# Kernel tuning notes

Measured on AMD Instinct MI355X. Metric: run time of the kernel, lower is better.

The kernel has to match this reference:

```python
import jax, jax.numpy as jnp
import numpy as np

BPTT, BSZ, NTOKEN = 32, 32, 2000
NINP, NHID = 1024, 256


def setup_inputs() -> dict:
    key = jax.random.key(0)
    ks = jax.random.split(key, 8)
    s = 0.1  # matches uniform(-0.1, 0.1) init scale
    return {
        "input": jax.random.normal(ks[0], (BPTT, BSZ, NTOKEN), jnp.float32),
        "b": jax.random.normal(ks[1], (BSZ, NHID), jnp.float32),
        "RBF_w": jax.random.uniform(ks[2], (NINP, NTOKEN), jnp.float32, -s, s),
        "RBF_b": jnp.zeros((NINP,), jnp.float32),
        "emb_w": jax.random.uniform(ks[3], (NHID, NINP), jnp.float32, -s, s),
        "emb_b": jnp.zeros((NHID,), jnp.float32),
        "wfef_w": jax.random.uniform(ks[4], (NHID * NHID, NHID), jnp.float32, -s, s),
        "wfef_b": jnp.zeros((NHID * NHID,), jnp.float32),
        "dec_w": jax.random.uniform(ks[5], (NTOKEN, NHID), jnp.float32, -s, s),
        "dec_b": jnp.zeros((NTOKEN,), jnp.float32),
    }


def reference(input, b, RBF_w, RBF_b, emb_w, emb_b, wfef_w, wfef_b, dec_w, dec_b):
    bptt, bsz, ntoken = input.shape
    nhid = b.shape[1]
    ninp = RBF_w.shape[0]
    rbf_scale = np.float32(np.sqrt(2.0) / np.sqrt(ninp))
    # random Fourier features: cos(RBF(x)) * sqrt(2/ninp)
    encoded = jnp.cos(input @ RBF_w.T + RBF_b) * rbf_scale      # [bptt,bsz,ninp]
    obs = encoded @ emb_w.T + emb_b                              # [bptt,bsz,nhid]

    def step(b_t, obs_t):
        # per-sample transition matrix from current state
        W = (b_t @ wfef_w.T + wfef_b).reshape(bsz, nhid, nhid)   # [bsz,nhid,nhid]
        bn = jnp.einsum('brc,bc->br', W, obs_t)                  # [bsz,nhid]
        bn = bn / jnp.sqrt(jnp.sum(bn * bn, axis=1, keepdims=True))
        out = bn @ dec_w.T + dec_b                               # [bsz,ntoken]
        return bn, out

    b_final, outputs = jax.lax.scan(step, b, obs)                # outputs: [bptt,bsz,ntoken]
    return outputs, b_final
```

## Files before the change

### kernel.cpp

```cpp
#include <hip/hip_runtime.h>
#include <hip/hip_fp16.h>
#include <math.h>

typedef _Float16 half_t;
typedef __attribute__((ext_vector_type(2))) _Float16 f16x2;
typedef __attribute__((ext_vector_type(4))) _Float16 f16x4;
typedef __attribute__((ext_vector_type(8))) _Float16 f16x8;
typedef __attribute__((ext_vector_type(4))) float f32x4;

#define BPTT 32
#define BSZ 32
#define NTOK 2000
#define NTOKP 2048
#define NINP 1024
#define NHID 256
#define TB 1024
#define NH2 65536
#define TCH 16

__device__ __forceinline__ int swz(int row, int hoff) {
  return (row * 32 + hoff) ^ ((row & 7) << 3);
}


__global__ void cvt_split_pad_k(const float* __restrict__ in, half_t* __restrict__ hi,
                                half_t* __restrict__ lo, int cols) {
  int idx = blockIdx.x * 256 + threadIdx.x;
  int r = idx >> 11, c = idx & 2047;
  float v = (c < cols) ? in[(size_t)r * cols + c] : 0.f;
  half_t h = (half_t)v;
  hi[idx] = h;
  lo[idx] = (half_t)(v - (float)h);
}

__global__ void cvt_half_k(const float* __restrict__ in, half_t* __restrict__ out, int n) {
  int idx = blockIdx.x * 256 + threadIdx.x;
  if (idx < n) out[idx] = (half_t)in[idx];
}

__global__ void cvt_pad_rows_k(const float* __restrict__ in, half_t* __restrict__ out,
                               int rows_valid) {
  int idx = blockIdx.x * 256 + threadIdx.x;
  int r = idx >> 8, c = idx & 255;
  float v = (r < rows_valid) ? in[(size_t)r * 256 + c] : 0.f;
  out[idx] = (half_t)v;
}

__global__ void permute_wfef_k(const float* __restrict__ wfef, half_t* __restrict__ wwt) {
  __shared__ float tile[32][33];
  int r = blockIdx.x, cb = blockIdx.y, hb = blockIdx.z;
  int tx = threadIdx.x, ty = threadIdx.y;
#pragma unroll
  for (int ii = 0; ii < 4; ii++) {
    int cl = ty + ii * 8;
    tile[cl][tx] = wfef[((size_t)(r * 256 + cb * 32 + cl)) * 256 + hb * 32 + tx];
  }
  __syncthreads();
#pragma unroll
  for (int ii = 0; ii < 4; ii++) {
    int hl = ty + ii * 8;
    wwt[((size_t)(hb * 32 + hl) * 256 + r) * 256 + cb * 32 + tx] = (half_t)tile[tx][hl];
  }
}

template <int EP>
__device__ __forceinline__ void gemm128_body(const half_t* __restrict__ A,
                                             const half_t* __restrict__ B,
                                             void* __restrict__ C,
                                             const float* __restrict__ bias, int K,
                                             int ldc, int nvalid, int row0, int col0) {
  __shared__ half_t As[128 * 32];
  __shared__ half_t Bs[128 * 32];
  const int tid = threadIdx.x;
  const int lane = tid & 63, wave = tid >> 6;
  const int wr = wave >> 1, wc = wave & 1;
  const int srow = tid >> 2, sseg = tid & 3;
  const size_t aoff = (size_t)(row0 + srow) * K + sseg * 8;
  const size_t boff = (size_t)(col0 + srow) * K + sseg * 8;
  const int fr = lane & 15, fq = lane >> 4;

  f32x4 acc[4][4];
#pragma unroll
  for (int m = 0; m < 4; m++)
#pragma unroll
    for (int n = 0; n < 4; n++) acc[m][n] = (f32x4)(0.0f);

  for (int k0 = 0; k0 < K; k0 += 32) {
    f16x8 a0 = *(const f16x8*)(A + aoff + k0);
    f16x8 a1 = *(const f16x8*)(A + aoff + (size_t)64 * K + k0);
    f16x8 b0 = *(const f16x8*)(B + boff + k0);
    f16x8 b1 = *(const f16x8*)(B + boff + (size_t)64 * K + k0);
    __syncthreads();
    *(f16x8*)(As + swz(srow, sseg * 8)) = a0;
    *(f16x8*)(As + swz(srow + 64, sseg * 8)) = a1;
    *(f16x8*)(Bs + swz(srow, sseg * 8)) = b0;
    *(f16x8*)(Bs + swz(srow + 64, sseg * 8)) = b1;
    __syncthreads();
    f16x8 af[4], bf[4];
#pragma unroll
    for (int m = 0; m < 4; m++)
      af[m] = *(const f16x8*)(As + swz(wr * 64 + m * 16 + fr, fq * 8));
#pragma unroll
    for (int n = 0; n < 4; n++)
      bf[n] = *(const f16x8*)(Bs + swz(wc * 64 + n * 16 + fr, fq * 8));
#pragma unroll
    for (int m = 0; m < 4; m++)
#pragma unroll
      for (int n = 0; n < 4; n++)
        acc[m][n] = __builtin_amdgcn_mfma_f32_16x16x32_f16(af[m], bf[n], acc[m][n], 0, 0, 0);
  }

#pragma unroll
  for (int m = 0; m < 4; m++) {
#pragma unroll
    for (int n = 0; n < 4; n++) {
#pragma unroll
      for (int j = 0; j < 4; j++) {
        int gr = row0 + wr * 64 + m * 16 + fq * 4 + j;
        int gc = col0 + wc * 64 + n * 16 + fr;
        float v = acc[m][n][j];
        if (EP == 0) {
          ((half_t*)C)[(size_t)gr * ldc + gc] = (half_t)v;
        } else if (EP == 1) {
          ((half_t*)C)[(size_t)gr * ldc + gc] = (half_t)(v + bias[gc]);
        } else if (EP == 2) {
          ((float*)C)[(size_t)gr * ldc + gc] = v;
        } else {
          if (gc < nvalid) ((float*)C)[(size_t)gr * ldc + gc] = v + bias[gc];
        }
      }
    }
  }
}

template <int EP>
__global__ __launch_bounds__(256) void gemm128_k(const half_t* __restrict__ A,
                                                 const half_t* __restrict__ B,
                                                 void* __restrict__ C,
                                                 const float* __restrict__ bias, int K,
                                                 int ldc, int nvalid) {
  gemm128_body<EP>(A, B, C, bias, K, ldc, nvalid, blockIdx.x * 128, blockIdx.y * 128);
}

__global__ __launch_bounds__(256) void gemm_m_k(const half_t* __restrict__ A,
                                                const half_t* __restrict__ B,
                                                half_t* __restrict__ C) {
  int id = blockIdx.x;
  int c = id & 7, k = id >> 3;
  int bx = k & 3, by = c + 8 * (k >> 2);
  gemm128_body<0>(A, B, (void*)C, nullptr, 256, NH2, 0, bx * 128, by * 128);
}

__global__ __launch_bounds__(256) void gemm1_splitk_k(
    const half_t* __restrict__ Ahi, const half_t* __restrict__ Alo,
    const half_t* __restrict__ Bhi, const half_t* __restrict__ Blo,
    float* __restrict__ P) {
  __shared__ half_t Ash[128 * 32];
  __shared__ half_t Asl[128 * 32];
  __shared__ half_t Bsh[64 * 32];
  __shared__ half_t Bsl[64 * 32];
  const int id = blockIdx.x;
  const int kp = id & 3, r2 = id >> 2;
  const int bx = r2 & 7, by = r2 >> 3;
  const int row0 = bx * 128, col0 = by * 64, koff = kp * 512;
  const int tid = threadIdx.x;
  const int lane = tid & 63, wave = tid >> 6;
  const int wr = wave >> 1, wc = wave & 1;
  const int srow = tid >> 2, sseg = tid & 3;
  const size_t aoff = (size_t)(row0 + srow) * NTOKP + koff + sseg * 8;
  const size_t boff = (size_t)(col0 + srow) * NTOKP + koff + sseg * 8;
  const int fr = lane & 15, fq = lane >> 4;

  f32x4 acc[4][2];
#pragma unroll
  for (int m = 0; m < 4; m++)
#pragma unroll
    for (int n = 0; n < 2; n++) acc[m][n] = (f32x4)(0.0f);

  for (int k0 = 0; k0 < 512; k0 += 32) {
    f16x8 ah0 = *(const f16x8*)(Ahi + aoff + k0);
    f16x8 ah1 = *(const f16x8*)(Ahi + aoff + (size_t)64 * NTOKP + k0);
    f16x8 al0 = *(const f16x8*)(Alo + aoff + k0);
    f16x8 al1 = *(const f16x8*)(Alo + aoff + (size_t)64 * NTOKP + k0);
    f16x8 bh0 = *(const f16x8*)(Bhi + boff + k0);
    f16x8 bl0 = *(const f16x8*)(Blo + boff + k0);
    __syncthreads();
    *(f16x8*)(Ash + swz(srow, sseg * 8)) = ah0;
    *(f16x8*)(Ash + swz(srow + 64, sseg * 8)) = ah1;
    *(f16x8*)(Asl + swz(srow, sseg * 8)) = al0;
    *(f16x8*)(Asl + swz(srow + 64, sseg * 8)) = al1;
    *(f16x8*)(Bsh + swz(srow, sseg * 8)) = bh0;
    *(f16x8*)(Bsl + swz(srow, sseg * 8)) = bl0;
    __syncthreads();
    f16x8 afh[4], afl[4], bfh[2], bfl[2];
#pragma unroll
    for (int m = 0; m < 4; m++) {
      afh[m] = *(const f16x8*)(Ash + swz(wr * 64 + m * 16 + fr, fq * 8));
      afl[m] = *(const f16x8*)(Asl + swz(wr * 64 + m * 16 + fr, fq * 8));
    }
#pragma unroll
    for (int n = 0; n < 2; n++) {
      bfh[n] = *(const f16x8*)(Bsh + swz(wc * 32 + n * 16 + fr, fq * 8));
      bfl[n] = *(const f16x8*)(Bsl + swz(wc * 32 + n * 16 + fr, fq * 8));
    }
#pragma unroll
    for (int m = 0; m < 4; m++)
#pragma unroll
      for (int n = 0; n < 2; n++) {
        acc[m][n] = __builtin_amdgcn_mfma_f32_16x16x32_f16(afh[m], bfh[n], acc[m][n], 0, 0, 0);
        acc[m][n] = __builtin_amdgcn_mfma_f32_16x16x32_f16(afl[m], bfh[n], acc[m][n], 0, 0, 0);
        acc[m][n] = __builtin_amdgcn_mfma_f32_16x16x32_f16(afh[m], bfl[n], acc[m][n], 0, 0, 0);
      }
  }

  float* Pk = P + (size_t)kp * (NINP * (size_t)TB);
#pragma unroll
  for (int m = 0; m < 4; m++) {
#pragma unroll
    for (int n = 0; n < 2; n++) {
#pragma unroll
      for (int j = 0; j < 4; j++) {
        int gr = row0 + wr * 64 + m * 16 + fq * 4 + j;
        int gc = col0 + wc * 32 + n * 16 + fr;
        Pk[(size_t)gr * NINP + gc] = acc[m][n][j];
      }
    }
  }
}

__global__ void rbf_combine_k(const float* __restrict__ P, const float* __restrict__ bias,
                              half_t* __restrict__ C) {
  int idx = blockIdx.x * 256 + threadIdx.x;
  int e0 = idx * 4;
  int col = e0 & (NINP - 1);
  f32x4 s = *(const f32x4*)(P + e0);
  s += *(const f32x4*)(P + (size_t)1 * TB * NINP + e0);
  s += *(const f32x4*)(P + (size_t)2 * TB * NINP + e0);
  s += *(const f32x4*)(P + (size_t)3 * TB * NINP + e0);
  const float RBF_SCALE = 0.04419417382415922f;
  f16x4 o;
#pragma unroll
  for (int j = 0; j < 4; j++) o[j] = (half_t)(cosf(s[j] + bias[col + j]) * RBF_SCALE);
  *(f16x4*)(C + e0) = o;
}

__global__ __launch_bounds__(1024, 4) void scan_seg_k(
    const half_t* __restrict__ Mc, const float* __restrict__ V, int t0,
    const float* __restrict__ bin, float* __restrict__ bstate,
    half_t* __restrict__ BN, float* __restrict__ bfinal) {
  __shared__ float Vs[TCH][256];
  __shared__ float partial[16][260];
  __shared__ __align__(16) unsigned bh2[128];
  __shared__ float red[4];
  const int b = blockIdx.x, tid = threadIdx.x;
  const int hh = tid >> 6;
  const int rv = tid & 63;

  *(f32x4*)&Vs[hh][rv * 4] =
      *(const f32x4*)(V + ((size_t)(t0 + hh) * 32 + b) * 256 + rv * 4);
  if (tid < 128) {
    const float* bs = bin + b * 256 + tid * 2;
    union { f16x2 h; unsigned u; } z;
    z.h[0] = (half_t)bs[0];
    z.h[1] = (half_t)bs[1];
    bh2[tid] = z.u;
  }

  const half_t* mbase = Mc + (size_t)b * NH2 + (hh * 16) * 256 + rv * 4;
  f16x4 cur[16], nxt[16];
#pragma unroll
  for (int k = 0; k < 16; k++) cur[k] = *(const f16x4*)(mbase + k * 256);
  __syncthreads();

  for (int tt = 0; tt < TCH; tt++) {
    const int tn = (tt < TCH - 1) ? tt + 1 : TCH - 1;
    const half_t* mb2 = mbase + (size_t)tn * 32 * NH2;
#pragma unroll
    for (int k = 0; k < 16; k++) nxt[k] = *(const f16x4*)(mb2 + k * 256);

    uint4 bq0 = *(const uint4*)&bh2[hh * 8];
    uint4 bq1 = *(const uint4*)&bh2[hh * 8 + 4];
    half_t hv[16];
    *(uint4*)&hv[0] = bq0;
    *(uint4*)&hv[8] = bq1;

    float a0 = 0.f, a1 = 0.f, a2 = 0.f, a3 = 0.f;
#pragma unroll
    for (int k = 0; k < 16; k++) {
      a0 += (float)cur[k][0] * (float)hv[k];
      a1 += (float)cur[k][1] * (float)hv[k];
      a2 += (float)cur[k][2] * (float)hv[k];
      a3 += (float)cur[k][3] * (float)hv[k];
    }
    f32x4 av = {a0, a1, a2, a3};
    *(f32x4*)&partial[hh][rv * 4] = av;
    __syncthreads();

    float s = 0.f;
    if (tid < 256) {
#pragma unroll
      for (int g = 0; g < 16; g++) s += partial[g][tid];
      s += Vs[tt][tid];
      float sq = s * s;
#pragma unroll
      for (int o = 32; o > 0; o >>= 1) sq += __shfl_xor(sq, o);
      if ((tid & 63) == 0) red[tid >> 6] = sq;
    }
    __syncthreads();
    if (tid < 256) {
      float sumsq = red[0] + red[1] + red[2] + red[3];
      float bnv = s / sqrtf(sumsq);
      float bnv_hi = __shfl_down(bnv, 1);
      if (!(tid & 1)) {
        union { f16x2 h; unsigned u; } z;
        z.h[0] = (half_t)bnv;
        z.h[1] = (half_t)bnv_hi;
        bh2[tid >> 1] = z.u;
        *(unsigned*)(BN + ((size_t)(t0 + tt) * 32 + b) * 256 + tid) = z.u;
      }
      if (tt == TCH - 1) bstate[b * 256 + tid] = bnv;
      if (t0 + tt == BPTT - 1) bfinal[b * 256 + tid] = bnv;
    }
    __syncthreads();
#pragma unroll
    for (int k = 0; k < 16; k++) cur[k] = nxt[k];
  }
}


extern "C" void kernel_launch(void* const* d_in, const int* in_sizes, int n_in,
                              void* d_out, int out_size, void* d_ws, size_t ws_size,
                              hipStream_t stream) {
  const float* input = (const float*)d_in[0];
  const float* b0 = (const float*)d_in[1];
  const float* RBF_w = (const float*)d_in[2];
  const float* RBF_b = (const float*)d_in[3];
  const float* emb_w = (const float*)d_in[4];
  const float* emb_b = (const float*)d_in[5];
  const float* wfef_w = (const float*)d_in[6];
  const float* wfef_b = (const float*)d_in[7];
  const float* dec_w = (const float*)d_in[8];
  const float* dec_b = (const float*)d_in[9];

  char* ws = (char*)d_ws;
  size_t off = 0;
  auto alloc = [&](size_t bytes) {
    void* p = ws + off;
    off += (bytes + 255) & ~(size_t)255;
    return p;
  };
  half_t* A1hi = (half_t*)alloc((size_t)TB * NTOKP * 2);
  half_t* A1lo = (half_t*)alloc((size_t)TB * NTOKP * 2);
  half_t* B1hi = (half_t*)alloc((size_t)NINP * NTOKP * 2);
  half_t* B1lo = (half_t*)alloc((size_t)NINP * NTOKP * 2);
  half_t* encA = (half_t*)alloc((size_t)TB * NINP * 2);
  half_t* B2 = (half_t*)alloc((size_t)NHID * NINP * 2);
  half_t* obsA = (half_t*)alloc((size_t)TB * NHID * 2);
  half_t* WBh = (half_t*)alloc((size_t)NHID * NHID * 2);
  half_t* B4 = (half_t*)alloc((size_t)2048 * NHID * 2);
  float* Vbuf = (float*)alloc((size_t)TB * NHID * 4);
  half_t* BN = (half_t*)alloc((size_t)TB * NHID * 2);
  float* bstate = (float*)alloc((size_t)BSZ * NHID * 4);
  half_t* WWT = (half_t*)alloc((size_t)NH2 * NHID * 2);
  half_t* Mmat = (half_t*)alloc((size_t)TB * NH2 * 2);
  if (off > ws_size) return;

  float* Pk = (float*)Mmat;

  float* outp = (float*)d_out;
  float* bfinal = outp + (size_t)TB * NTOK;

  cvt_split_pad_k<<<(TB * NTOKP) / 256, 256, 0, stream>>>(input, A1hi, A1lo, NTOK);
  cvt_split_pad_k<<<(NINP * NTOKP) / 256, 256, 0, stream>>>(RBF_w, B1hi, B1lo, NTOK);
  cvt_half_k<<<(NHID * NINP) / 256, 256, 0, stream>>>(emb_w, B2, NHID * NINP);
  cvt_half_k<<<(NHID * NHID) / 256, 256, 0, stream>>>(wfef_b, WBh, NHID * NHID);
  cvt_pad_rows_k<<<(2048 * NHID) / 256, 256, 0, stream>>>(dec_w, B4, NTOK);
  permute_wfef_k<<<dim3(256, 8, 8), dim3(32, 8), 0, stream>>>(wfef_w, WWT);

  gemm1_splitk_k<<<512, 256, 0, stream>>>(A1hi, A1lo, B1hi, B1lo, Pk);
  rbf_combine_k<<<(TB * NINP / 4) / 256, 256, 0, stream>>>(Pk, RBF_b, encA);
  gemm128_k<1><<<dim3(8, 2), 256, 0, stream>>>(encA, B2, obsA, emb_b, NINP, NHID, 0);
  gemm128_k<2><<<dim3(8, 2), 256, 0, stream>>>(obsA, WBh, Vbuf, nullptr, NHID, NHID, 0);

  for (int tc = 0; tc < BPTT / TCH; tc++) {
    const int t0 = tc * TCH;
    gemm_m_k<<<2048, 256, 0, stream>>>(obsA + (size_t)t0 * 32 * NHID, WWT,
                                       Mmat + (size_t)t0 * 32 * NH2);
    scan_seg_k<<<32, 1024, 0, stream>>>(Mmat + (size_t)t0 * 32 * NH2, Vbuf, t0,
                                        (t0 == 0) ? b0 : bstate, bstate, BN, bfinal);
  }

  gemm128_k<3><<<dim3(8, 16), 256, 0, stream>>>(BN, B4, outp, dec_b, NHID, NTOK, NTOK);
}
```

Before: 261.1 us.

## Overlap second-chunk M gemm with first scan segment in fused kernel

Runs the scan over the first time chunk in the same launch as the per-token M-matrix GEMM for the second chunk, with block index choosing the role, so the serial scan overlaps with the large GEMM. The M GEMM now uses 256x256 tiles with 1024-thread blocks, and the scan loads f16x8 vectors with split-half accumulation plus a shuffle. The five conversion kernels are merged into two to cut launch count. The scan blocks compete with GEMM blocks for CUs, and both roles share the same dynamic LDS sizing, which may limit occupancy.

```diff
diff --git a/kernel.cpp b/kernel.cpp
--- a/kernel.cpp
+++ b/kernel.cpp
@@ -17,33 +17,43 @@
 #define TB 1024
 #define NH2 65536
 #define TCH 16
+#define SCAN_LDS 33552
 
 __device__ __forceinline__ int swz(int row, int hoff) {
   return (row * 32 + hoff) ^ ((row & 7) << 3);
 }
 
 
-__global__ void cvt_split_pad_k(const float* __restrict__ in, half_t* __restrict__ hi,
-                                half_t* __restrict__ lo, int cols) {
-  int idx = blockIdx.x * 256 + threadIdx.x;
+__global__ void cvt_split2_k(const float* __restrict__ inA, half_t* __restrict__ hiA,
+                             half_t* __restrict__ loA, const float* __restrict__ inB,
+                             half_t* __restrict__ hiB, half_t* __restrict__ loB) {
+  int bid = blockIdx.x;
+  const float* src;
+  half_t *hi, *lo;
+  int idx;
+  if (bid < 8192) {
+    src = inA; hi = hiA; lo = loA; idx = bid * 256 + threadIdx.x;
+  } else {
+    src = inB; hi = hiB; lo = loB; idx = (bid - 8192) * 256 + threadIdx.x;
+  }
   int r = idx >> 11, c = idx & 2047;
-  float v = (c < cols) ? in[(size_t)r * cols + c] : 0.f;
+  float v = (c < NTOK) ? src[(size_t)r * NTOK + c] : 0.f;
   half_t h = (half_t)v;
   hi[idx] = h;
   lo[idx] = (half_t)(v - (float)h);
 }
 
-__global__ void cvt_half_k(const float* __restrict__ in, half_t* __restrict__ out, int n) {
-  int idx = blockIdx.x * 256 + threadIdx.x;
-  if (idx < n) out[idx] = (half_t)in[idx];
-}
-
-__global__ void cvt_pad_rows_k(const float* __restrict__ in, half_t* __restrict__ out,
-                               int rows_valid) {
-  int idx = blockIdx.x * 256 + threadIdx.x;
-  int r = idx >> 8, c = idx & 255;
-  float v = (r < rows_valid) ? in[(size_t)r * 256 + c] : 0.f;
-  out[idx] = (half_t)v;
+__global__ void cvt_misc_k(const float* __restrict__ emb_w,
+                           const float* __restrict__ wfef_b,
+                           const float* __restrict__ dec_w, half_t* __restrict__ B2,
+                           half_t* __restrict__ WBh, half_t* __restrict__ B4) {
+  int i = blockIdx.x * 256 + threadIdx.x;
+  if (i < 262144) { B2[i] = (half_t)emb_w[i]; return; }
+  i -= 262144;
+  if (i < 65536) { WBh[i] = (half_t)wfef_b[i]; return; }
+  i -= 65536;
+  int r = i >> 8, c = i & 255;
+  B4[i] = (half_t)((r < NTOK) ? dec_w[(size_t)r * 256 + c] : 0.f);
 }
 
 __global__ void permute_wfef_k(const float* __restrict__ wfef, half_t* __restrict__ wwt) {
@@ -64,16 +74,17 @@
 }
 
 template <int EP>
-__device__ __forceinline__ void gemm128_body(const half_t* __restrict__ A,
-                                             const half_t* __restrict__ B,
-                                             void* __restrict__ C,
-                                             const float* __restrict__ bias, int K,
-                                             int ldc, int nvalid, int row0, int col0) {
+__global__ __launch_bounds__(256) void gemm128_k(const half_t* __restrict__ A,
+                                                 const half_t* __restrict__ B,
+                                                 void* __restrict__ C,
+                                                 const float* __restrict__ bias, int K,
+                                                 int ldc, int nvalid) {
   __shared__ half_t As[128 * 32];
   __shared__ half_t Bs[128 * 32];
   const int tid = threadIdx.x;
   const int lane = tid & 63, wave = tid >> 6;
   const int wr = wave >> 1, wc = wave & 1;
+  const int row0 = blockIdx.x * 128, col0 = blockIdx.y * 128;
   const int srow = tid >> 2, sseg = tid & 3;
   const size_t aoff = (size_t)(row0 + srow) * K + sseg * 8;
   const size_t boff = (size_t)(col0 + srow) * K + sseg * 8;
@@ -119,9 +130,7 @@
         int gr = row0 + wr * 64 + m * 16 + fq * 4 + j;
         int gc = col0 + wc * 64 + n * 16 + fr;
         float v = acc[m][n][j];
-        if (EP == 0) {
-          ((half_t*)C)[(size_t)gr * ldc + gc] = (half_t)v;
-        } else if (EP == 1) {
+        if (EP == 1) {
           ((half_t*)C)[(size_t)gr * ldc + gc] = (half_t)(v + bias[gc]);
         } else if (EP == 2) {
           ((float*)C)[(size_t)gr * ldc + gc] = v;
@@ -133,22 +142,178 @@
   }
 }
 
-template <int EP>
-__global__ __launch_bounds__(256) void gemm128_k(const half_t* __restrict__ A,
-                                                 const half_t* __restrict__ B,
-                                                 void* __restrict__ C,
-                                                 const float* __restrict__ bias, int K,
-                                                 int ldc, int nvalid) {
-  gemm128_body<EP>(A, B, C, bias, K, ldc, nvalid, blockIdx.x * 128, blockIdx.y * 128);
-}
-
-__global__ __launch_bounds__(256) void gemm_m_k(const half_t* __restrict__ A,
-                                                const half_t* __restrict__ B,
-                                                half_t* __restrict__ C) {
+__device__ __forceinline__ void gemm256_body(const half_t* __restrict__ A,
+                                             const half_t* __restrict__ B,
+                                             half_t* __restrict__ C, int K, size_t ldc,
+                                             int row0, int col0, char* smem) {
+  half_t* As = (half_t*)smem;
+  half_t* Bs = (half_t*)(smem + 16384);
+  const int tid = threadIdx.x;
+  const int lane = tid & 63, wave = tid >> 6;
+  const int wr = wave >> 2, wc = wave & 3;
+  const int srow = tid >> 2, sseg = tid & 3;
+  const size_t aoff = (size_t)(row0 + srow) * K + sseg * 8;
+  const size_t boff = (size_t)(col0 + srow) * K + sseg * 8;
+  const int fr = lane & 15, fq = lane >> 4;
+
+  f32x4 acc[4][4];
+#pragma unroll
+  for (int m = 0; m < 4; m++)
+#pragma unroll
+    for (int n = 0; n < 4; n++) acc[m][n] = (f32x4)(0.0f);
+
+  for (int k0 = 0; k0 < K; k0 += 32) {
+    f16x8 a0 = *(const f16x8*)(A + aoff + k0);
+    f16x8 b0 = *(const f16x8*)(B + boff + k0);
+    __syncthreads();
+    *(f16x8*)(As + swz(srow, sseg * 8)) = a0;
+    *(f16x8*)(Bs + swz(srow, sseg * 8)) = b0;
+    __syncthreads();
+    f16x8 af[4], bf[4];
+#pragma unroll
+    for (int m = 0; m < 4; m++)
+      af[m] = *(const f16x8*)(As + swz(wr * 64 + m * 16 + fr, fq * 8));
+#pragma unroll
+    for (int n = 0; n < 4; n++)
+      bf[n] = *(const f16x8*)(Bs + swz(wc * 64 + n * 16 + fr, fq * 8));
+#pragma unroll
+    for (int m = 0; m < 4; m++)
+#pragma unroll
+      for (int n = 0; n < 4; n++)
+        acc[m][n] = __builtin_amdgcn_mfma_f32_16x16x32_f16(af[m], bf[n], acc[m][n], 0, 0, 0);
+  }
+
+#pragma unroll
+  for (int m = 0; m < 4; m++)
+#pragma unroll
+    for (int n = 0; n < 4; n++)
+#pragma unroll
+      for (int j = 0; j < 4; j++) {
+        int gr = row0 + wr * 64 + m * 16 + fq * 4 + j;
+        int gc = col0 + wc * 64 + n * 16 + fr;
+        C[(size_t)gr * ldc + gc] = (half_t)acc[m][n][j];
+      }
+}
+
+__device__ void scan_body(const half_t* __restrict__ Mc, const float* __restrict__ V,
+                          int t0, const float* __restrict__ bin,
+                          float* __restrict__ bstate, half_t* __restrict__ BN,
+                          float* __restrict__ bfinal, int b, char* smem) {
+  float(*Vs)[256] = (float(*)[256])smem;
+  float(*partial)[260] = (float(*)[260])(smem + 16384);
+  unsigned* bh2 = (unsigned*)(smem + 33024);
+  float* red = (float*)(smem + 33536);
+  const int tid = threadIdx.x;
+  const int hh = tid >> 6, lane = tid & 63;
+  const int hpar = lane >> 5, r8 = (lane & 31) * 8;
+
+  *(f32x4*)&Vs[hh][lane * 4] =
+      *(const f32x4*)(V + ((size_t)(t0 + hh) * 32 + b) * 256 + lane * 4);
+  if (tid < 128) {
+    const float* bs = bin + b * 256 + tid * 2;
+    union { f16x2 h; unsigned u; } z;
+    z.h[0] = (half_t)bs[0];
+    z.h[1] = (half_t)bs[1];
+    bh2[tid] = z.u;
+  }
+
+  const half_t* mbase = Mc + (size_t)b * NH2 + (size_t)(hh * 16 + hpar) * 256 + r8;
+  f16x8 cur[8], nxt[8];
+#pragma unroll
+  for (int k = 0; k < 8; k++) cur[k] = *(const f16x8*)(mbase + k * 512);
+  __syncthreads();
+
+  for (int tt = 0; tt < TCH; tt++) {
+    const int tn = (tt < TCH - 1) ? tt + 1 : TCH - 1;
+    const half_t* mb2 = mbase + (size_t)tn * 32 * NH2;
+#pragma unroll
+    for (int k = 0; k < 8; k++) nxt[k] = *(const f16x8*)(mb2 + k * 512);
+
+    uint4 q0 = *(const uint4*)&bh2[hh * 8];
+    uint4 q1 = *(const uint4*)&bh2[hh * 8 + 4];
+    unsigned bu[8] = {q0.x, q0.y, q0.z, q0.w, q1.x, q1.y, q1.z, q1.w};
+    const int sh = hpar * 16;
+    half_t hv[8];
+#pragma unroll
+    for (int k = 0; k < 8; k++)
+      hv[k] = __builtin_bit_cast(half_t, (unsigned short)(bu[k] >> sh));
+
+    float a[8] = {0.f, 0.f, 0.f, 0.f, 0.f, 0.f, 0.f, 0.f};
+#pragma unroll
+    for (int k = 0; k < 8; k++)
+#pragma unroll
+      for (int j = 0; j < 8; j++) a[j] += (float)cur[k][j] * (float)hv[k];
+#pragma unroll
+    for (int j = 0; j < 8; j++) a[j] += __shfl_xor(a[j], 32);
+    f32x4 st = hpar ? (f32x4){a[4], a[5], a[6], a[7]} : (f32x4){a[0], a[1], a[2], a[3]};
+    *(f32x4*)&partial[hh][r8 + hpar * 4] = st;
+    __syncthreads();
+
+    float s = 0.f;
+    if (tid < 256) {
+#pragma unroll
+      for (int g = 0; g < 16; g++) s += partial[g][tid];
+      s += Vs[tt][tid];
+      float sq = s * s;
+#pragma unroll
+      for (int o = 32; o > 0; o >>= 1) sq += __shfl_xor(sq, o);
+      if ((tid & 63) == 0) red[tid >> 6] = sq;
+    }
+    __syncthreads();
+    if (tid < 256) {
+      float sumsq = red[0] + red[1] + red[2] + red[3];
+      float bnv = s / sqrtf(sumsq);
+      float bnv_hi = __shfl_down(bnv, 1);
+      if (!(tid & 1)) {
+        union { f16x2 h; unsigned u; } z;
+        z.h[0] = (half_t)bnv;
+        z.h[1] = (half_t)bnv_hi;
+        bh2[tid >> 1] = z.u;
+        *(unsigned*)(BN + ((size_t)(t0 + tt) * 32 + b) * 256 + tid) = z.u;
+      }
+      if (tt == TCH - 1) bstate[b * 256 + tid] = bnv;
+      if (t0 + tt == BPTT - 1) bfinal[b * 256 + tid] = bnv;
+    }
+    __syncthreads();
+#pragma unroll
+    for (int k = 0; k < 8; k++) cur[k] = nxt[k];
+  }
+}
+
+
+__global__ __launch_bounds__(1024, 4) void gemm256_k(const half_t* __restrict__ A,
+                                                     const half_t* __restrict__ B,
+                                                     half_t* __restrict__ C) {
+  extern __shared__ char smem[];
   int id = blockIdx.x;
   int c = id & 7, k = id >> 3;
-  int bx = k & 3, by = c + 8 * (k >> 2);
-  gemm128_body<0>(A, B, (void*)C, nullptr, 256, NH2, 0, bx * 128, by * 128);
+  int bx = k & 1, by = c + 8 * (k >> 1);
+  gemm256_body(A, B, C, 256, NH2, bx * 256, by * 256, smem);
+}
+
+__global__ __launch_bounds__(1024, 4) void fused_scan_gemm_k(
+    const half_t* __restrict__ Mc, const float* __restrict__ V,
+    const float* __restrict__ bin, float* __restrict__ bstate,
+    half_t* __restrict__ BN, float* __restrict__ bfinal,
+    const half_t* __restrict__ Ag, const half_t* __restrict__ Bg,
+    half_t* __restrict__ Cg) {
+  extern __shared__ char smem[];
+  if (blockIdx.x < 32) {
+    scan_body(Mc, V, 0, bin, bstate, BN, bfinal, blockIdx.x, smem);
+  } else {
+    int id = blockIdx.x - 32;
+    int c = id & 7, k = id >> 3;
+    int bx = k & 1, by = c + 8 * (k >> 1);
+    gemm256_body(Ag, Bg, Cg, 256, NH2, bx * 256, by * 256, smem);
+  }
+}
+
+__global__ __launch_bounds__(1024, 4) void scan_only_k(
+    const half_t* __restrict__ Mc, const float* __restrict__ V, int t0,
+    const float* __restrict__ bin, float* __restrict__ bstate,
+    half_t* __restrict__ BN, float* __restrict__ bfinal) {
+  extern __shared__ char smem[];
+  scan_body(Mc, V, t0, bin, bstate, BN, bfinal, blockIdx.x, smem);
 }
 
 __global__ __launch_bounds__(256) void gemm1_splitk_k(
@@ -215,17 +380,15 @@
 
   float* Pk = P + (size_t)kp * (NINP * (size_t)TB);
 #pragma unroll
-  for (int m = 0; m < 4; m++) {
-#pragma unroll
-    for (int n = 0; n < 2; n++) {
+  for (int m = 0; m < 4; m++)
+#pragma unroll
+    for (int n = 0; n < 2; n++)
 #pragma unroll
       for (int j = 0; j < 4; j++) {
         int gr = row0 + wr * 64 + m * 16 + fq * 4 + j;
         int gc = col0 + wc * 32 + n * 16 + fr;
         Pk[(size_t)gr * NINP + gc] = acc[m][n][j];
       }
-    }
-  }
 }
 
 __global__ void rbf_combine_k(const float* __restrict__ P, const float* __restrict__ bias,
@@ -242,89 +405,6 @@
 #pragma unroll
   for (int j = 0; j < 4; j++) o[j] = (half_t)(cosf(s[j] + bias[col + j]) * RBF_SCALE);
   *(f16x4*)(C + e0) = o;
-}
-
-__global__ __launch_bounds__(1024, 4) void scan_seg_k(
-    const half_t* __restrict__ Mc, const float* __restrict__ V, int t0,
-    const float* __restrict__ bin, float* __restrict__ bstate,
-    half_t* __restrict__ BN, float* __restrict__ bfinal) {
-  __shared__ float Vs[TCH][256];
-  __shared__ float partial[16][260];
-  __shared__ __align__(16) unsigned bh2[128];
-  __shared__ float red[4];
-  const int b = blockIdx.x, tid = threadIdx.x;
-  const int hh = tid >> 6;
-  const int rv = tid & 63;
-
-  *(f32x4*)&Vs[hh][rv * 4] =
-      *(const f32x4*)(V + ((size_t)(t0 + hh) * 32 + b) * 256 + rv * 4);
-  if (tid < 128) {
-    const float* bs = bin + b * 256 + tid * 2;
-    union { f16x2 h; unsigned u; } z;
-    z.h[0] = (half_t)bs[0];
-    z.h[1] = (half_t)bs[1];
-    bh2[tid] = z.u;
-  }
-
-  const half_t* mbase = Mc + (size_t)b * NH2 + (hh * 16) * 256 + rv * 4;
-  f16x4 cur[16], nxt[16];
-#pragma unroll
-  for (int k = 0; k < 16; k++) cur[k] = *(const f16x4*)(mbase + k * 256);
-  __syncthreads();
-
-  for (int tt = 0; tt < TCH; tt++) {
-    const int tn = (tt < TCH - 1) ? tt + 1 : TCH - 1;
-    const half_t* mb2 = mbase + (size_t)tn * 32 * NH2;
-#pragma unroll
-    for (int k = 0; k < 16; k++) nxt[k] = *(const f16x4*)(mb2 + k * 256);
-
-    uint4 bq0 = *(const uint4*)&bh2[hh * 8];
-    uint4 bq1 = *(const uint4*)&bh2[hh * 8 + 4];
-    half_t hv[16];
-    *(uint4*)&hv[0] = bq0;
-    *(uint4*)&hv[8] = bq1;
-
-    float a0 = 0.f, a1 = 0.f, a2 = 0.f, a3 = 0.f;
-#pragma unroll
-    for (int k = 0; k < 16; k++) {
-      a0 += (float)cur[k][0] * (float)hv[k];
-      a1 += (float)cur[k][1] * (float)hv[k];
-      a2 += (float)cur[k][2] * (float)hv[k];
-      a3 += (float)cur[k][3] * (float)hv[k];
-    }
-    f32x4 av = {a0, a1, a2, a3};
-    *(f32x4*)&partial[hh][rv * 4] = av;
-    __syncthreads();
-
-    float s = 0.f;
-    if (tid < 256) {
-#pragma unroll
-      for (int g = 0; g < 16; g++) s += partial[g][tid];
-      s += Vs[tt][tid];
-      float sq = s * s;
-#pragma unroll
-      for (int o = 32; o > 0; o >>= 1) sq += __shfl_xor(sq, o);
-      if ((tid & 63) == 0) red[tid >> 6] = sq;
-    }
-    __syncthreads();
-    if (tid < 256) {
-      float sumsq = red[0] + red[1] + red[2] + red[3];
-      float bnv = s / sqrtf(sumsq);
-      float bnv_hi = __shfl_down(bnv, 1);
-      if (!(tid & 1)) {
-        union { f16x2 h; unsigned u; } z;
-        z.h[0] = (half_t)bnv;
-        z.h[1] = (half_t)bnv_hi;
-        bh2[tid >> 1] = z.u;
-        *(unsigned*)(BN + ((size_t)(t0 + tt) * 32 + b) * 256 + tid) = z.u;
-      }
-      if (tt == TCH - 1) bstate[b * 256 + tid] = bnv;
-      if (t0 + tt == BPTT - 1) bfinal[b * 256 + tid] = bnv;
-    }
-    __syncthreads();
-#pragma unroll
-    for (int k = 0; k < 16; k++) cur[k] = nxt[k];
-  }
 }
 
 
@@ -370,11 +450,8 @@
   float* outp = (float*)d_out;
   float* bfinal = outp + (size_t)TB * NTOK;
 
-  cvt_split_pad_k<<<(TB * NTOKP) / 256, 256, 0, stream>>>(input, A1hi, A1lo, NTOK);
-  cvt_split_pad_k<<<(NINP * NTOKP) / 256, 256, 0, stream>>>(RBF_w, B1hi, B1lo, NTOK);
-  cvt_half_k<<<(NHID * NINP) / 256, 256, 0, stream>>>(emb_w, B2, NHID * NINP);
-  cvt_half_k<<<(NHID * NHID) / 256, 256, 0, stream>>>(wfef_b, WBh, NHID * NHID);
-  cvt_pad_rows_k<<<(2048 * NHID) / 256, 256, 0, stream>>>(dec_w, B4, NTOK);
+  cvt_split2_k<<<16384, 256, 0, stream>>>(input, A1hi, A1lo, RBF_w, B1hi, B1lo);
+  cvt_misc_k<<<3328, 256, 0, stream>>>(emb_w, wfef_b, dec_w, B2, WBh, B4);
   permute_wfef_k<<<dim3(256, 8, 8), dim3(32, 8), 0, stream>>>(wfef_w, WWT);
 
   gemm1_splitk_k<<<512, 256, 0, stream>>>(A1hi, A1lo, B1hi, B1lo, Pk);
@@ -382,13 +459,12 @@
   gemm128_k<1><<<dim3(8, 2), 256, 0, stream>>>(encA, B2, obsA, emb_b, NINP, NHID, 0);
   gemm128_k<2><<<dim3(8, 2), 256, 0, stream>>>(obsA, WBh, Vbuf, nullptr, NHID, NHID, 0);
 
-  for (int tc = 0; tc < BPTT / TCH; tc++) {
-    const int t0 = tc * TCH;
-    gemm_m_k<<<2048, 256, 0, stream>>>(obsA + (size_t)t0 * 32 * NHID, WWT,
-                                       Mmat + (size_t)t0 * 32 * NH2);
-    scan_seg_k<<<32, 1024, 0, stream>>>(Mmat + (size_t)t0 * 32 * NH2, Vbuf, t0,
-                                        (t0 == 0) ? b0 : bstate, bstate, BN, bfinal);
-  }
+  gemm256_k<<<512, 1024, 32768, stream>>>(obsA, WWT, Mmat);
+  fused_scan_gemm_k<<<544, 1024, SCAN_LDS, stream>>>(
+      Mmat, Vbuf, b0, bstate, BN, bfinal, obsA + (size_t)512 * NHID, WWT,
+      Mmat + (size_t)512 * NH2);
+  scan_only_k<<<32, 1024, SCAN_LDS, stream>>>(Mmat + (size_t)512 * NH2, Vbuf, TCH,
+                                              bstate, bstate, BN, bfinal);
 
   gemm128_k<3><<<dim3(8, 16), 256, 0, stream>>>(BN, B4, outp, dec_b, NHID, NTOK, NTOK);
 }
```

Result: slower. 296.7 us (+13.6%).
